# Performance work log

Hardware: AMD Instinct MI355X
Metric: run time of the kernel (lower is better)

The kernel has to match this reference:

```python
import jax, jax.numpy as jnp
import numpy as np

B, T, EMB, NDIM = 8, 2048, 1024, 1024


def setup_inputs() -> dict:
    key = jax.random.key(0)
    k1, k2, k3, k4 = jax.random.split(key, 4)
    X = jax.random.normal(k1, (B, T, EMB), dtype=jnp.float32)
    # Linear(emb, ndim, bias=False); stored as [emb, ndim] so projection is X @ W.
    scale = 1.0 / np.sqrt(EMB)
    Wq = jax.random.normal(k2, (EMB, NDIM), dtype=jnp.float32) * scale
    Wk = jax.random.normal(k3, (EMB, NDIM), dtype=jnp.float32) * scale
    Wv = jax.random.normal(k4, (EMB, NDIM), dtype=jnp.float32) * scale
    return {"X": X, "Wq": Wq, "Wk": Wk, "Wv": Wv}


def reference(X, Wq, Wk, Wv):
    ndim = Wq.shape[-1]
    T_ = X.shape[1]
    Q = X @ Wq  # [B,T,ndim]
    K = X @ Wk  # [B,T,ndim]
    V = X @ Wv  # [B,T,ndim]
    # scores[b,t,s] = Q[b,t] . K[b,s], scaled by ndim^-0.5
    scores = jnp.einsum("btd,bsd->bts", Q, K) * (ndim ** -0.5)
    mask = jnp.tril(jnp.ones((T_, T_), dtype=bool))  # causal lower-triangular
    scores = jnp.where(mask, scores, -jnp.inf)
    # NOTE: source uses F.softmax(..., dim=1) -> normalize over the QUERY axis
    # (columns of the [T,T] matrix), not the usual key axis. Replicated faithfully.
    probs = jax.nn.softmax(scores, axis=1)
    # dropout is identity in eval / p=0 deterministic baseline
    return probs @ V  # [B,T,ndim]
```

## Files before the change

kernel.cpp:

```cpp
#include <hip/hip_runtime.h>
#include <hip/hip_bf16.h>

#define B_   8
#define T_   2048
#define EMB_ 1024
#define ND_  1024
#define NTB  16
#define NPAIR 136
#define NTB2 8
#define NPAIR2 36

typedef __attribute__((ext_vector_type(8))) short   bf8_t;
typedef __attribute__((ext_vector_type(4))) float   f32x4;

__device__ __forceinline__ unsigned short f2bf(float f) {
  union { float f; unsigned int u; } c; c.f = f;
  unsigned int u = c.u;
  unsigned int r = (u + 0x7FFFu + ((u >> 16) & 1u)) >> 16;
  return (unsigned short)r;
}

__device__ __forceinline__ float bf2f(unsigned short b) {
  union { unsigned int u; float f; } c; c.u = ((unsigned int)b) << 16;
  return c.f;
}

__device__ __forceinline__ void gload_lds16(const unsigned short* g, unsigned short* l) {
  __builtin_amdgcn_global_load_lds(
      (const __attribute__((address_space(1))) unsigned int*)g,
      (__attribute__((address_space(3))) unsigned int*)l,
      16, 0, 0);
}

__device__ __forceinline__ void tri_decode(int p, int& tblk, int& sblk) {
  int t = (int)((sqrtf(8.0f * (float)p + 1.0f) - 1.0f) * 0.5f);
  while ((t + 1) * (t + 2) / 2 <= p) ++t;
  while (t * (t + 1) / 2 > p) --t;
  tblk = t;
  sblk = p - t * (t + 1) / 2;
}

#define SB0() __builtin_amdgcn_sched_barrier(0)
#define BAR() __builtin_amdgcn_s_barrier()

__device__ __forceinline__ void stage_half(const unsigned short* __restrict__ g, int lda,
                                           unsigned short* lhalf, int wave, int lane) {
  const int r3 = lane >> 3, c3 = lane & 7;
  const int colsw = ((c3 ^ r3) << 3);
#pragma unroll
  for (int j = 0; j < 2; ++j) {
    const int row = wave * 8 + r3 + 64 * j;
    gload_lds16(g + (size_t)row * lda + colsw, lhalf + wave * 512 + j * 4096);
  }
}

__device__ __forceinline__ bf8_t read_frag(const unsigned short* half, int r, int ks, int lane) {
  const int col = (((ks) << 5) + ((lane >> 4) << 3)) ^ ((r & 7) << 3);
  return *(const bf8_t*)(half + r * 64 + col);
}

__global__ void __launch_bounds__(256) cvt_x_kernel(const float* __restrict__ in,
                                                    unsigned short* __restrict__ out) {
  const int i = (blockIdx.x * 256 + threadIdx.x) * 4;
  float4 v = *(const float4*)(in + i);
  ushort4 o = make_ushort4(f2bf(v.x), f2bf(v.y), f2bf(v.z), f2bf(v.w));
  *(ushort4*)(out + i) = o;
}

__global__ void __launch_bounds__(256) transpose_w_kernel(const float* __restrict__ W,
                                                          unsigned short* __restrict__ Wt,
                                                          float cscale) {
  __shared__ unsigned short tile[32][33];
  const int n0 = blockIdx.x * 32, k0 = blockIdx.y * 32;
  const int tx = threadIdx.x & 31, ty = threadIdx.x >> 5;
#pragma unroll
  for (int r = 0; r < 32; r += 8) {
    float v = W[(size_t)(k0 + ty + r) * ND_ + n0 + tx];
    tile[tx][ty + r] = f2bf(v * cscale);
  }
  __syncthreads();
#pragma unroll
  for (int r = 0; r < 32; r += 8) {
    Wt[(size_t)(n0 + ty + r) * EMB_ + k0 + tx] = tile[ty + r][tx];
  }
}

#define LDSA(d, h) (lds256 + ((d) * 2 + (h)) * 8192)
#define LDSB(d, h) (lds256 + 32768 + ((d) * 2 + (h)) * 8192)

#define MFMA_QUAD(MB, AF, AOFF) do { \
  __builtin_amdgcn_s_setprio(1); \
  _Pragma("unroll") \
  for (int mi = 0; mi < 2; ++mi) \
    _Pragma("unroll") \
    for (int nf = 0; nf < 4; ++nf) \
      _Pragma("unroll") \
      for (int ks = 0; ks < 2; ++ks) \
        acc[(MB) * 2 + mi][nf] = __builtin_amdgcn_mfma_f32_16x16x32_bf16( \
            (AF)[(AOFF) + mi][ks], bfr[nf][ks], acc[(MB) * 2 + mi][nf], 0, 0, 0); \
  __builtin_amdgcn_s_setprio(0); \
} while (0)

#define GEMM256_LOOP(ABASE, BBASE, LDK) \
  stage_half((ABASE),                           (LDK), LDSA(0, 0), wave, lane); \
  stage_half((ABASE) + (size_t)128 * (LDK),     (LDK), LDSA(0, 1), wave, lane); \
  stage_half((BBASE),                           (LDK), LDSB(0, 0), wave, lane); \
  stage_half((BBASE) + (size_t)128 * (LDK),     (LDK), LDSB(0, 1), wave, lane); \
  stage_half((BBASE) + 64,                      (LDK), LDSB(1, 0), wave, lane); \
  stage_half((BBASE) + (size_t)128 * (LDK) + 64,(LDK), LDSB(1, 1), wave, lane); \
  stage_half((ABASE) + 64,                      (LDK), LDSA(1, 0), wave, lane); \
  asm volatile("s_waitcnt vmcnt(6)" ::: "memory"); \
  SB0(); BAR(); SB0(); \
  for (int t = 0; t < 16; ++t) { \
    const int d = t & 1; \
    const unsigned short* Ah = LDSA(d, wm); \
    const unsigned short* Bh = LDSB(d, wn >> 1); \
    bf8_t bfr[4][2], af[4][2]; \
    _Pragma("unroll") \
    for (int nf = 0; nf < 4; ++nf) \
      _Pragma("unroll") \
      for (int ks = 0; ks < 2; ++ks) bfr[nf][ks] = read_frag(Bh, brow + nf * 16, ks, lane); \
    _Pragma("unroll") \
    for (int mf = 0; mf < 4; ++mf) \
      _Pragma("unroll") \
      for (int ks = 0; ks < 2; ++ks) af[mf][ks] = read_frag(Ah, arow + mf * 16, ks, lane); \
    SB0(); \
    if (t < 15) stage_half((ABASE) + (size_t)128 * (LDK) + (size_t)(t + 1) * 64, (LDK), LDSA(d ^ 1, 1), wave, lane); \
    SB0(); BAR(); SB0(); \
    MFMA_QUAD(0, af, 0); \
    SB0(); \
    asm volatile("s_waitcnt lgkmcnt(0)" ::: "memory"); \
    SB0(); BAR(); SB0(); \
    if (t < 14) stage_half((BBASE) + (size_t)(t + 2) * 64, (LDK), LDSB(d, 0), wave, lane); \
    SB0(); BAR(); SB0(); \
    MFMA_QUAD(1, af, 2); \
    SB0(); BAR(); SB0(); \
    bf8_t af2[4][2]; \
    _Pragma("unroll") \
    for (int mf = 0; mf < 4; ++mf) \
      _Pragma("unroll") \
      for (int ks = 0; ks < 2; ++ks) af2[mf][ks] = read_frag(Ah, arow + (mf + 4) * 16, ks, lane); \
    SB0(); \
    if (t < 14) stage_half((BBASE) + (size_t)128 * (LDK) + (size_t)(t + 2) * 64, (LDK), LDSB(d, 1), wave, lane); \
    SB0(); BAR(); SB0(); \
    MFMA_QUAD(2, af2, 0); \
    SB0(); \
    asm volatile("s_waitcnt lgkmcnt(0)" ::: "memory"); \
    SB0(); BAR(); SB0(); \
    if (t < 14) stage_half((ABASE) + (size_t)(t + 2) * 64, (LDK), LDSA(d, 0), wave, lane); \
    if (t < 14)      { asm volatile("s_waitcnt vmcnt(6)" ::: "memory"); } \
    else if (t == 14){ asm volatile("s_waitcnt vmcnt(0)" ::: "memory"); } \
    SB0(); BAR(); SB0(); \
    MFMA_QUAD(3, af2, 2); \
    SB0(); BAR(); SB0(); \
  }

template <int OUTMODE>
__global__ void __launch_bounds__(512, 2)
gemm_xw256_kernel(const unsigned short* __restrict__ A,
                  const unsigned short* __restrict__ Bt,
                  unsigned short* __restrict__ C) {
  extern __shared__ unsigned short lds256[];
  const int tid = threadIdx.x, lane = tid & 63, wave = tid >> 6;
  const int wm = wave >> 2, wn = wave & 3;
  const int m0 = blockIdx.y * 256, n0 = blockIdx.x * 256;
  const unsigned short* Ab = A + (size_t)m0 * EMB_;
  const unsigned short* Bb = Bt + (size_t)n0 * EMB_;
  f32x4 acc[8][4];
#pragma unroll
  for (int i = 0; i < 8; ++i)
#pragma unroll
    for (int j = 0; j < 4; ++j)
#pragma unroll
      for (int q = 0; q < 4; ++q) acc[i][j][q] = 0.f;
  const int arow = lane & 15;
  const int brow = (wn & 1) * 64 + (lane & 15);

  GEMM256_LOOP(Ab, Bb, EMB_)

  const int cc = lane & 15, cr4 = (lane >> 4) << 2;
#pragma unroll
  for (int mf = 0; mf < 8; ++mf)
#pragma unroll
    for (int nf = 0; nf < 4; ++nf)
#pragma unroll
      for (int q = 0; q < 4; ++q) {
        const int row = m0 + wm * 128 + mf * 16 + cr4 + q;
        const int col = n0 + wn * 64 + nf * 16 + cc;
        const unsigned short val = f2bf(acc[mf][nf][q]);
        if (OUTMODE == 0) {
          C[(size_t)row * ND_ + col] = val;
        } else {
          const int bb = row >> 11, tt = row & 2047;
          C[((size_t)bb * ND_ + col) * T_ + tt] = val;
        }
      }
}

__global__ void __launch_bounds__(512, 2)
scoretile256_kernel(const unsigned short* __restrict__ Qb,
                    const unsigned short* __restrict__ Kb,
                    unsigned short* __restrict__ Sb,
                    float* __restrict__ pm,
                    float* __restrict__ pl) {
  extern __shared__ unsigned short lds256[];
  int tr, sr;
  tri_decode(blockIdx.x, tr, sr);
  const int b = blockIdx.y;
  const int tid = threadIdx.x, lane = tid & 63, wave = tid >> 6;
  const int wm = wave >> 2, wn = wave & 3;
  const int t0 = tr * 256, s0 = sr * 256;
  const unsigned short* Ab = Qb + ((size_t)b * T_ + t0) * ND_;
  const unsigned short* Bb = Kb + ((size_t)b * T_ + s0) * ND_;
  f32x4 acc[8][4];
#pragma unroll
  for (int i = 0; i < 8; ++i)
#pragma unroll
    for (int j = 0; j < 4; ++j)
#pragma unroll
      for (int q = 0; q < 4; ++q) acc[i][j][q] = 0.f;
  const int arow = lane & 15;
  const int brow = (wn & 1) * 64 + (lane & 15);

  GEMM256_LOOP(Ab, Bb, ND_)

  const int cc = lane & 15, cr4 = (lane >> 4) << 2;
  const bool diag = (tr == sr);
  unsigned short* Sbase = Sb + (size_t)b * T_ * T_;
  float rm[4], rl[4];
#pragma unroll
  for (int nf = 0; nf < 4; ++nf) { rm[nf] = -1e30f; rl[nf] = 0.f; }
#pragma unroll
  for (int mf = 0; mf < 8; ++mf)
#pragma unroll
    for (int nf = 0; nf < 4; ++nf)
#pragma unroll
      for (int q = 0; q < 4; ++q) {
        const int t = t0 + wm * 128 + mf * 16 + cr4 + q;
        const int s = s0 + wn * 64 + nf * 16 + cc;
        const bool ok = !diag || (t >= s);
        const unsigned short bv = ok ? f2bf(acc[mf][nf][q]) : (unsigned short)0;
        Sbase[(size_t)t * T_ + s] = bv;
        if (ok) {
          const float v = bf2f(bv);
          const float mm = fmaxf(rm[nf], v);
          rl[nf] = rl[nf] * __expf(rm[nf] - mm) + __expf(v - mm);
          rm[nf] = mm;
        }
      }
#pragma unroll
  for (int nf = 0; nf < 4; ++nf) {
#pragma unroll
    for (int off = 16; off < 64; off <<= 1) {
      const float om = __shfl_xor(rm[nf], off);
      const float ol = __shfl_xor(rl[nf], off);
      const float mm = fmaxf(rm[nf], om);
      rl[nf] = rl[nf] * __expf(rm[nf] - mm) + ol * __expf(om - mm);
      rm[nf] = mm;
    }
  }
  __syncthreads();
  float* red = (float*)lds256;
  if (lane < 16) {
#pragma unroll
    for (int nf = 0; nf < 4; ++nf) {
      red[((wm * 4 + wn) * 4 + nf) * 16 + lane] = rm[nf];
      red[512 + ((wm * 4 + wn) * 4 + nf) * 16 + lane] = rl[nf];
    }
  }
  __syncthreads();
  if (wm == 0 && lane < 16) {
    const size_t base = (((size_t)b * NTB2 + sr) * NTB2 + tr) * 256;
#pragma unroll
    for (int nf = 0; nf < 4; ++nf) {
      const float m0v = red[((0 * 4 + wn) * 4 + nf) * 16 + lane];
      const float l0v = red[512 + ((0 * 4 + wn) * 4 + nf) * 16 + lane];
      const float m1v = red[((1 * 4 + wn) * 4 + nf) * 16 + lane];
      const float l1v = red[512 + ((1 * 4 + wn) * 4 + nf) * 16 + lane];
      const float mm = fmaxf(m0v, m1v);
      const float ll = l0v * __expf(m0v - mm) + l1v * __expf(m1v - mm);
      pm[base + wn * 64 + nf * 16 + lane] = mm;
      pl[base + wn * 64 + nf * 16 + lane] = ll;
    }
  }
}

__global__ void __launch_bounds__(256) colreduce_kernel(const float* __restrict__ pm,
                                                        const float* __restrict__ pl,
                                                        float* __restrict__ colmax,
                                                        float* __restrict__ colinv) {
  const int sr = blockIdx.x, b = blockIdx.y, c = threadIdx.x;
  float m = -1e30f, l = 0.f;
  for (int tr = sr; tr < NTB2; ++tr) {
    const size_t base = (((size_t)b * NTB2 + sr) * NTB2 + tr) * 256;
    const float om = pm[base + c], ol = pl[base + c];
    const float mm = fmaxf(m, om);
    l = l * __expf(m - mm) + ol * __expf(om - mm);
    m = mm;
  }
  colmax[(size_t)b * T_ + sr * 256 + c] = m;
  colinv[(size_t)b * T_ + sr * 256 + c] = 1.0f / l;
}

__global__ void __launch_bounds__(256) pscale_kernel(unsigned short* __restrict__ Pb,
                                                     const float* __restrict__ colmax,
                                                     const float* __restrict__ colinv) {
  int tblk, sblk;
  tri_decode(blockIdx.x, tblk, sblk);
  const int b = blockIdx.y;
  const int s0 = sblk * 128, t0 = tblk * 128;
  const int tid = threadIdx.x;
  const int col8 = (tid & 15) * 8;
  const int rbase = tid >> 4;
  unsigned short* Pbase = Pb + (size_t)b * T_ * T_;
  float ms[8], inv[8];
#pragma unroll
  for (int j = 0; j < 8; ++j) {
    ms[j]  = colmax[(size_t)b * T_ + s0 + col8 + j];
    inv[j] = colinv[(size_t)b * T_ + s0 + col8 + j];
  }
  const bool diag = (tblk == sblk);
  for (int r = rbase; r < 128; r += 16) {
    const int t = t0 + r;
    unsigned short* p = Pbase + (size_t)t * T_ + s0 + col8;
    bf8_t v = *(bf8_t*)p;
#pragma unroll
    for (int j = 0; j < 8; ++j) {
      float pv = 0.f;
      if (!diag || t >= s0 + col8 + j) {
        pv = __expf(bf2f((unsigned short)v[j]) - ms[j]) * inv[j];
      }
      v[j] = (short)f2bf(pv);
    }
    *(bf8_t*)p = v;
  }
}

#define MFMA_Q8(MB) do { \
  __builtin_amdgcn_s_setprio(1); \
  _Pragma("unroll") \
  for (int nf = 0; nf < 4; ++nf) \
    _Pragma("unroll") \
    for (int ks = 0; ks < 2; ++ks) \
      acc[(MB)][nf] = __builtin_amdgcn_mfma_f32_16x16x32_bf16( \
          af[(MB)][ks], bfr[nf][ks], acc[(MB)][nf], 0, 0, 0); \
  __builtin_amdgcn_s_setprio(0); \
} while (0)

__device__ __forceinline__ void pv_segment(const unsigned short* __restrict__ Ab,
                                           const unsigned short* __restrict__ Bb,
                                           float* __restrict__ Cb,
                                           int ktiles, unsigned short* lds256,
                                           int lane, int wave) {
  const int wm = wave >> 2, wn = wave & 3;
  const int arow = lane & 15;
  f32x4 acc[4][4];
#pragma unroll
  for (int i = 0; i < 4; ++i)
#pragma unroll
    for (int j = 0; j < 4; ++j)
#pragma unroll
      for (int q = 0; q < 4; ++q) acc[i][j][q] = 0.f;

  stage_half(Ab,                           T_, lds256,                     wave, lane);
  stage_half(Bb,                           T_, lds256 + 16384,             wave, lane);
  stage_half(Bb + (size_t)128 * T_,        T_, lds256 + 16384 + 8192,      wave, lane);
  stage_half(Ab + 64,                      T_, lds256 + 8192,              wave, lane);
  stage_half(Bb + 64,                      T_, lds256 + 16384 + 2 * 8192,  wave, lane);
  stage_half(Bb + (size_t)128 * T_ + 64,   T_, lds256 + 16384 + 3 * 8192,  wave, lane);
  asm volatile("s_waitcnt vmcnt(6)" ::: "memory");
  SB0(); BAR(); SB0();

  for (int t = 0; t < ktiles; ++t) {
    const int d = t & 1;
    const unsigned short* Ah = lds256 + d * 8192;
    const unsigned short* Bh = lds256 + 16384 + (d * 2 + (wn >> 1)) * 8192;
    bf8_t bfr[4][2], af[4][2];
#pragma unroll
    for (int nf = 0; nf < 4; ++nf)
#pragma unroll
      for (int ks = 0; ks < 2; ++ks)
        bfr[nf][ks] = read_frag(Bh, (wn & 1) * 64 + nf * 16 + arow, ks, lane);
#pragma unroll
    for (int mf = 0; mf < 4; ++mf)
#pragma unroll
      for (int ks = 0; ks < 2; ++ks)
        af[mf][ks] = read_frag(Ah, wm * 64 + mf * 16 + arow, ks, lane);
    SB0(); BAR(); SB0();
    MFMA_Q8(0);
    SB0();
    asm volatile("s_waitcnt lgkmcnt(0)" ::: "memory");
    SB0(); BAR(); SB0();
    if (t < ktiles - 2) stage_half(Ab + (size_t)(t + 2) * 64, T_, lds256 + d * 8192, wave, lane);
    SB0(); BAR(); SB0();
    MFMA_Q8(1);
    SB0(); BAR(); SB0();
    if (t < ktiles - 2) stage_half(Bb + (size_t)(t + 2) * 64, T_, lds256 + 16384 + (d * 2) * 8192, wave, lane);
    SB0(); BAR(); SB0();
    MFMA_Q8(2);
    SB0(); BAR(); SB0();
    if (t < ktiles - 2) stage_half(Bb + (size_t)128 * T_ + (size_t)(t + 2) * 64, T_, lds256 + 16384 + (d * 2 + 1) * 8192, wave, lane);
    if (t < ktiles - 2)      { asm volatile("s_waitcnt vmcnt(6)" ::: "memory"); }
    else if (t == ktiles - 2){ asm volatile("s_waitcnt vmcnt(0)" ::: "memory"); }
    SB0(); BAR(); SB0();
    MFMA_Q8(3);
    SB0(); BAR(); SB0();
  }

  const int cc = lane & 15, cr4 = (lane >> 4) << 2;
#pragma unroll
  for (int mf = 0; mf < 4; ++mf)
#pragma unroll
    for (int nf = 0; nf < 4; ++nf)
#pragma unroll
      for (int q = 0; q < 4; ++q) {
        const int row = wm * 64 + mf * 16 + cr4 + q;
        const int col = wn * 64 + nf * 16 + cc;
        Cb[(size_t)row * ND_ + col] = acc[mf][nf][q];
      }
}

__global__ void __launch_bounds__(512, 2)
gemm_pv256_kernel(const unsigned short* __restrict__ Pb,
                  const unsigned short* __restrict__ Vt,
                  float* __restrict__ out) {
  extern __shared__ unsigned short lds256[];
  const int pair = blockIdx.x;
  const int ncol = blockIdx.y;
  const int b = blockIdx.z;
  const int tid = threadIdx.x, lane = tid & 63, wave = tid >> 6;
  const int tbs[2] = {pair, 15 - pair};
#pragma unroll
  for (int si = 0; si < 2; ++si) {
    const int tb = tbs[si];
    const int ktiles = 2 * tb + 2;
    pv_segment(Pb + (size_t)b * T_ * T_ + (size_t)tb * 128 * T_,
               Vt + (size_t)b * ND_ * T_ + (size_t)ncol * 256 * T_,
               out + (size_t)b * T_ * ND_ + (size_t)tb * 128 * ND_ + ncol * 256,
               ktiles, lds256, lane, wave);
  }
}

extern "C" void kernel_launch(void* const* d_in, const int* in_sizes, int n_in,
                              void* d_out, int out_size, void* d_ws, size_t ws_size,
                              hipStream_t stream) {
  const float* X  = (const float*)d_in[0];
  const float* Wq = (const float*)d_in[1];
  const float* Wk = (const float*)d_in[2];
  const float* Wv = (const float*)d_in[3];
  float* out = (float*)d_out;
  (void)in_sizes; (void)n_in; (void)out_size;

  char* ws = (char*)d_ws;
  size_t off = 0;
  auto alloc = [&](size_t bytes) {
    void* p = ws + off;
    off += (bytes + 255) & ~(size_t)255;
    return p;
  };
  unsigned short* Xb  = (unsigned short*)alloc((size_t)B_ * T_ * EMB_ * 2);
  unsigned short* Wtq = (unsigned short*)alloc((size_t)ND_ * EMB_ * 2);
  unsigned short* Wtk = (unsigned short*)alloc((size_t)ND_ * EMB_ * 2);
  unsigned short* Wtv = (unsigned short*)alloc((size_t)ND_ * EMB_ * 2);
  unsigned short* Qb  = (unsigned short*)alloc((size_t)B_ * T_ * ND_ * 2);
  unsigned short* Kb  = (unsigned short*)alloc((size_t)B_ * T_ * ND_ * 2);
  unsigned short* Vt  = (unsigned short*)alloc((size_t)B_ * ND_ * T_ * 2);
  float* colmax = (float*)alloc((size_t)B_ * T_ * 4);
  float* colinv = (float*)alloc((size_t)B_ * T_ * 4);
  float* pm     = (float*)alloc((size_t)B_ * NTB2 * NTB2 * 256 * 4);
  float* pl     = (float*)alloc((size_t)B_ * NTB2 * NTB2 * 256 * 4);
  unsigned short* Pb  = (unsigned short*)alloc((size_t)B_ * T_ * T_ * 2);
  if (off > ws_size) return;

  hipFuncSetAttribute((const void*)&gemm_xw256_kernel<0>,
                      hipFuncAttributeMaxDynamicSharedMemorySize, 131072);
  hipFuncSetAttribute((const void*)&gemm_xw256_kernel<1>,
                      hipFuncAttributeMaxDynamicSharedMemorySize, 131072);
  hipFuncSetAttribute((const void*)&scoretile256_kernel,
                      hipFuncAttributeMaxDynamicSharedMemorySize, 131072);
  hipFuncSetAttribute((const void*)&gemm_pv256_kernel,
                      hipFuncAttributeMaxDynamicSharedMemorySize, 98304);

  hipLaunchKernelGGL(cvt_x_kernel, dim3((B_ * T_ * EMB_) / 1024), dim3(256), 0, stream, X, Xb);
  hipLaunchKernelGGL(transpose_w_kernel, dim3(32, 32), dim3(256), 0, stream, Wq, Wtq, 0.03125f);
  hipLaunchKernelGGL(transpose_w_kernel, dim3(32, 32), dim3(256), 0, stream, Wk, Wtk, 1.0f);
  hipLaunchKernelGGL(transpose_w_kernel, dim3(32, 32), dim3(256), 0, stream, Wv, Wtv, 1.0f);
  hipLaunchKernelGGL((gemm_xw256_kernel<0>), dim3(ND_ / 256, (B_ * T_) / 256), dim3(512), 131072, stream, Xb, Wtq, Qb);
  hipLaunchKernelGGL((gemm_xw256_kernel<0>), dim3(ND_ / 256, (B_ * T_) / 256), dim3(512), 131072, stream, Xb, Wtk, Kb);
  hipLaunchKernelGGL((gemm_xw256_kernel<1>), dim3(ND_ / 256, (B_ * T_) / 256), dim3(512), 131072, stream, Xb, Wtv, Vt);
  hipLaunchKernelGGL(scoretile256_kernel, dim3(NPAIR2, B_), dim3(512), 131072, stream, Qb, Kb, Pb, pm, pl);
  hipLaunchKernelGGL(colreduce_kernel, dim3(NTB2, B_), dim3(256), 0, stream, pm, pl, colmax, colinv);
  hipLaunchKernelGGL(pscale_kernel, dim3(NPAIR, B_), dim3(256), 0, stream, Pb, colmax, colinv);
  hipLaunchKernelGGL(gemm_pv256_kernel, dim3(NTB2, ND_ / 256, B_), dim3(512), 98304, stream, Pb, Vt, out);
}
```

Measured before the change: 305.2 us.

## Stage GEMM epilogues through swizzled LDS, reschedule prefetches, remap grid order

The GEMM and score-tile epilogues now write bf16 results into swizzled LDS first and then store them to global memory as coalesced 16-byte vectors. This replaces scattered 2-byte stores, including the strided transposed V output. The prefetch schedule in the XW GEMM and PV loops is regrouped: A and B half-tiles are issued in pairs, waitcnt thresholds change, and all of the first A tile is loaded in the prologue. The score and PV grids are flattened so batch becomes the fastest-varying block index, which changes how blocks are spread across CUs and how they share cache. The risks are an extra barrier plus an LDS round trip, and heavier bursts of loads at each stage point.

After: 302.4 us. No clear change (-0.9%).

```diff
diff --git a/kernel.cpp b/kernel.cpp
--- a/kernel.cpp
+++ b/kernel.cpp
@@ -58,6 +58,8 @@
   const int col = (((ks) << 5) + ((lane >> 4) << 3)) ^ ((r & 7) << 3);
   return *(const bf8_t*)(half + r * 64 + col);
 }
+
+__device__ __forceinline__ int swz_ep(int x) { return ((x >> 1) & 7) << 4; }
 
 __global__ void __launch_bounds__(256) cvt_x_kernel(const float* __restrict__ in,
                                                     unsigned short* __restrict__ out) {
@@ -102,14 +104,15 @@
 } while (0)
 
 #define GEMM256_LOOP(ABASE, BBASE, LDK) \
-  stage_half((ABASE),                           (LDK), LDSA(0, 0), wave, lane); \
-  stage_half((ABASE) + (size_t)128 * (LDK),     (LDK), LDSA(0, 1), wave, lane); \
-  stage_half((BBASE),                           (LDK), LDSB(0, 0), wave, lane); \
-  stage_half((BBASE) + (size_t)128 * (LDK),     (LDK), LDSB(0, 1), wave, lane); \
-  stage_half((BBASE) + 64,                      (LDK), LDSB(1, 0), wave, lane); \
-  stage_half((BBASE) + (size_t)128 * (LDK) + 64,(LDK), LDSB(1, 1), wave, lane); \
-  stage_half((ABASE) + 64,                      (LDK), LDSA(1, 0), wave, lane); \
-  asm volatile("s_waitcnt vmcnt(6)" ::: "memory"); \
+  stage_half((ABASE),                             (LDK), LDSA(0, 0), wave, lane); \
+  stage_half((ABASE) + (size_t)128 * (LDK),       (LDK), LDSA(0, 1), wave, lane); \
+  stage_half((BBASE),                             (LDK), LDSB(0, 0), wave, lane); \
+  stage_half((BBASE) + (size_t)128 * (LDK),       (LDK), LDSB(0, 1), wave, lane); \
+  stage_half((BBASE) + 64,                        (LDK), LDSB(1, 0), wave, lane); \
+  stage_half((BBASE) + (size_t)128 * (LDK) + 64,  (LDK), LDSB(1, 1), wave, lane); \
+  stage_half((ABASE) + 64,                        (LDK), LDSA(1, 0), wave, lane); \
+  stage_half((ABASE) + (size_t)128 * (LDK) + 64,  (LDK), LDSA(1, 1), wave, lane); \
+  asm volatile("s_waitcnt vmcnt(8)" ::: "memory"); \
   SB0(); BAR(); SB0(); \
   for (int t = 0; t < 16; ++t) { \
     const int d = t & 1; \
@@ -124,14 +127,15 @@
     for (int mf = 0; mf < 4; ++mf) \
       _Pragma("unroll") \
       for (int ks = 0; ks < 2; ++ks) af[mf][ks] = read_frag(Ah, arow + mf * 16, ks, lane); \
-    SB0(); \
-    if (t < 15) stage_half((ABASE) + (size_t)128 * (LDK) + (size_t)(t + 1) * 64, (LDK), LDSA(d ^ 1, 1), wave, lane); \
     SB0(); BAR(); SB0(); \
     MFMA_QUAD(0, af, 0); \
     SB0(); \
     asm volatile("s_waitcnt lgkmcnt(0)" ::: "memory"); \
     SB0(); BAR(); SB0(); \
-    if (t < 14) stage_half((BBASE) + (size_t)(t + 2) * 64, (LDK), LDSB(d, 0), wave, lane); \
+    if (t < 14) { \
+      stage_half((BBASE) + (size_t)(t + 2) * 64,                     (LDK), LDSB(d, 0), wave, lane); \
+      stage_half((BBASE) + (size_t)128 * (LDK) + (size_t)(t + 2) * 64,(LDK), LDSB(d, 1), wave, lane); \
+    } \
     SB0(); BAR(); SB0(); \
     MFMA_QUAD(1, af, 2); \
     SB0(); BAR(); SB0(); \
@@ -140,20 +144,44 @@
     for (int mf = 0; mf < 4; ++mf) \
       _Pragma("unroll") \
       for (int ks = 0; ks < 2; ++ks) af2[mf][ks] = read_frag(Ah, arow + (mf + 4) * 16, ks, lane); \
-    SB0(); \
-    if (t < 14) stage_half((BBASE) + (size_t)128 * (LDK) + (size_t)(t + 2) * 64, (LDK), LDSB(d, 1), wave, lane); \
     SB0(); BAR(); SB0(); \
     MFMA_QUAD(2, af2, 0); \
     SB0(); \
     asm volatile("s_waitcnt lgkmcnt(0)" ::: "memory"); \
     SB0(); BAR(); SB0(); \
-    if (t < 14) stage_half((ABASE) + (size_t)(t + 2) * 64, (LDK), LDSA(d, 0), wave, lane); \
-    if (t < 14)      { asm volatile("s_waitcnt vmcnt(6)" ::: "memory"); } \
-    else if (t == 14){ asm volatile("s_waitcnt vmcnt(0)" ::: "memory"); } \
+    if (t < 14) { \
+      stage_half((ABASE) + (size_t)(t + 2) * 64,                     (LDK), LDSA(d, 0), wave, lane); \
+      stage_half((ABASE) + (size_t)128 * (LDK) + (size_t)(t + 2) * 64,(LDK), LDSA(d, 1), wave, lane); \
+      asm volatile("s_waitcnt vmcnt(8)" ::: "memory"); \
+    } else if (t == 14) { \
+      asm volatile("s_waitcnt vmcnt(0)" ::: "memory"); \
+    } \
     SB0(); BAR(); SB0(); \
     MFMA_QUAD(3, af2, 2); \
     SB0(); BAR(); SB0(); \
   }
+
+#define ACC_TO_LDS(TRANS, MASKED) do { \
+  _Pragma("unroll") \
+  for (int mf = 0; mf < 8; ++mf) \
+    _Pragma("unroll") \
+    for (int nf = 0; nf < 4; ++nf) \
+      _Pragma("unroll") \
+      for (int q = 0; q < 4; ++q) { \
+        const int r = wm * 128 + mf * 16 + cr4 + q; \
+        const int c = wn * 64 + nf * 16 + cc; \
+        unsigned short bv; \
+        if (MASKED) { \
+          const bool ok = !diag || (t0 + r >= s0 + c); \
+          bv = ok ? f2bf(acc[mf][nf][q]) : (unsigned short)0; \
+        } else { \
+          bv = f2bf(acc[mf][nf][q]); \
+        } \
+        const int byte = (TRANS) ? (c * 512 + ((r * 2) ^ swz_ep(c))) \
+                                 : (r * 512 + ((c * 2) ^ swz_ep(r))); \
+        lds256[byte >> 1] = bv; \
+      } \
+} while (0)
 
 template <int OUTMODE>
 __global__ void __launch_bounds__(512, 2)
@@ -179,22 +207,27 @@
   GEMM256_LOOP(Ab, Bb, EMB_)
 
   const int cc = lane & 15, cr4 = (lane >> 4) << 2;
-#pragma unroll
-  for (int mf = 0; mf < 8; ++mf)
-#pragma unroll
-    for (int nf = 0; nf < 4; ++nf)
-#pragma unroll
-      for (int q = 0; q < 4; ++q) {
-        const int row = m0 + wm * 128 + mf * 16 + cr4 + q;
-        const int col = n0 + wn * 64 + nf * 16 + cc;
-        const unsigned short val = f2bf(acc[mf][nf][q]);
-        if (OUTMODE == 0) {
-          C[(size_t)row * ND_ + col] = val;
-        } else {
-          const int bb = row >> 11, tt = row & 2047;
-          C[((size_t)bb * ND_ + col) * T_ + tt] = val;
-        }
-      }
+  const bool diag = false; const int t0 = 0, s0 = 0; (void)diag; (void)t0; (void)s0;
+  ACC_TO_LDS(OUTMODE == 1, false);
+  __syncthreads();
+  if (OUTMODE == 0) {
+#pragma unroll
+    for (int p = 0; p < 16; ++p) {
+      const int o = p * 8192 + tid * 16;
+      const int ri = o >> 9, cb = o & 511;
+      const bf8_t v = *(const bf8_t*)(lds256 + (((o & ~511) | (cb ^ swz_ep(ri))) >> 1));
+      *(bf8_t*)(C + (size_t)(m0 + ri) * ND_ + n0 + (cb >> 1)) = v;
+    }
+  } else {
+    const int bb = m0 >> 11, tt0 = m0 & 2047;
+#pragma unroll
+    for (int p = 0; p < 16; ++p) {
+      const int o = p * 8192 + tid * 16;
+      const int ci = o >> 9, rb = o & 511;
+      const bf8_t v = *(const bf8_t*)(lds256 + (((o & ~511) | (rb ^ swz_ep(ci))) >> 1));
+      *(bf8_t*)(C + ((size_t)bb * ND_ + n0 + ci) * T_ + tt0 + (rb >> 1)) = v;
+    }
+  }
 }
 
 __global__ void __launch_bounds__(512, 2)
@@ -204,9 +237,9 @@
                     float* __restrict__ pm,
                     float* __restrict__ pl) {
   extern __shared__ unsigned short lds256[];
+  const int b = blockIdx.x & 7;
   int tr, sr;
-  tri_decode(blockIdx.x, tr, sr);
-  const int b = blockIdx.y;
+  tri_decode(blockIdx.x >> 3, tr, sr);
   const int tid = threadIdx.x, lane = tid & 63, wave = tid >> 6;
   const int wm = wave >> 2, wn = wave & 3;
   const int t0 = tr * 256, s0 = sr * 256;
@@ -226,7 +259,6 @@
 
   const int cc = lane & 15, cr4 = (lane >> 4) << 2;
   const bool diag = (tr == sr);
-  unsigned short* Sbase = Sb + (size_t)b * T_ * T_;
   float rm[4], rl[4];
 #pragma unroll
   for (int nf = 0; nf < 4; ++nf) { rm[nf] = -1e30f; rl[nf] = 0.f; }
@@ -236,11 +268,11 @@
     for (int nf = 0; nf < 4; ++nf)
 #pragma unroll
       for (int q = 0; q < 4; ++q) {
-        const int t = t0 + wm * 128 + mf * 16 + cr4 + q;
-        const int s = s0 + wn * 64 + nf * 16 + cc;
-        const bool ok = !diag || (t >= s);
+        const int r = wm * 128 + mf * 16 + cr4 + q;
+        const int c = wn * 64 + nf * 16 + cc;
+        const bool ok = !diag || (t0 + r >= s0 + c);
         const unsigned short bv = ok ? f2bf(acc[mf][nf][q]) : (unsigned short)0;
-        Sbase[(size_t)t * T_ + s] = bv;
+        lds256[(r * 512 + ((c * 2) ^ swz_ep(r))) >> 1] = bv;
         if (ok) {
           const float v = bf2f(bv);
           const float mm = fmaxf(rm[nf], v);
@@ -248,6 +280,15 @@
           rm[nf] = mm;
         }
       }
+  __syncthreads();
+  unsigned short* Sbase = Sb + (size_t)b * T_ * T_;
+#pragma unroll
+  for (int p = 0; p < 16; ++p) {
+    const int o = p * 8192 + tid * 16;
+    const int ri = o >> 9, cb = o & 511;
+    const bf8_t v = *(const bf8_t*)(lds256 + (((o & ~511) | (cb ^ swz_ep(ri))) >> 1));
+    *(bf8_t*)(Sbase + (size_t)(t0 + ri) * T_ + s0 + (cb >> 1)) = v;
+  }
 #pragma unroll
   for (int nf = 0; nf < 4; ++nf) {
 #pragma unroll
@@ -391,15 +432,18 @@
     SB0();
     asm volatile("s_waitcnt lgkmcnt(0)" ::: "memory");
     SB0(); BAR(); SB0();
-    if (t < ktiles - 2) stage_half(Ab + (size_t)(t + 2) * 64, T_, lds256 + d * 8192, wave, lane);
+    if (t < ktiles - 2) {
+      stage_half(Ab + (size_t)(t + 2) * 64, T_, lds256 + d * 8192, wave, lane);
+      stage_half(Bb + (size_t)(t + 2) * 64, T_, lds256 + 16384 + (d * 2) * 8192, wave, lane);
+    }
     SB0(); BAR(); SB0();
     MFMA_Q8(1);
     SB0(); BAR(); SB0();
-    if (t < ktiles - 2) stage_half(Bb + (size_t)(t + 2) * 64, T_, lds256 + 16384 + (d * 2) * 8192, wave, lane);
+    if (t < ktiles - 2)
+      stage_half(Bb + (size_t)128 * T_ + (size_t)(t + 2) * 64, T_, lds256 + 16384 + (d * 2 + 1) * 8192, wave, lane);
     SB0(); BAR(); SB0();
     MFMA_Q8(2);
     SB0(); BAR(); SB0();
-    if (t < ktiles - 2) stage_half(Bb + (size_t)128 * T_ + (size_t)(t + 2) * 64, T_, lds256 + 16384 + (d * 2 + 1) * 8192, wave, lane);
     if (t < ktiles - 2)      { asm volatile("s_waitcnt vmcnt(6)" ::: "memory"); }
     else if (t == ktiles - 2){ asm volatile("s_waitcnt vmcnt(0)" ::: "memory"); }
     SB0(); BAR(); SB0();
@@ -425,9 +469,9 @@
                   const unsigned short* __restrict__ Vt,
                   float* __restrict__ out) {
   extern __shared__ unsigned short lds256[];
-  const int pair = blockIdx.x;
-  const int ncol = blockIdx.y;
-  const int b = blockIdx.z;
+  const int b = blockIdx.x & 7;
+  const int pair = (blockIdx.x >> 3) & 7;
+  const int ncol = blockIdx.x >> 6;
   const int tid = threadIdx.x, lane = tid & 63, wave = tid >> 6;
   const int tbs[2] = {pair, 15 - pair};
 #pragma unroll
@@ -488,8 +532,8 @@
   hipLaunchKernelGGL((gemm_xw256_kernel<0>), dim3(ND_ / 256, (B_ * T_) / 256), dim3(512), 131072, stream, Xb, Wtq, Qb);
   hipLaunchKernelGGL((gemm_xw256_kernel<0>), dim3(ND_ / 256, (B_ * T_) / 256), dim3(512), 131072, stream, Xb, Wtk, Kb);
   hipLaunchKernelGGL((gemm_xw256_kernel<1>), dim3(ND_ / 256, (B_ * T_) / 256), dim3(512), 131072, stream, Xb, Wtv, Vt);
-  hipLaunchKernelGGL(scoretile256_kernel, dim3(NPAIR2, B_), dim3(512), 131072, stream, Qb, Kb, Pb, pm, pl);
+  hipLaunchKernelGGL(scoretile256_kernel, dim3(NPAIR2 * B_), dim3(512), 131072, stream, Qb, Kb, Pb, pm, pl);
   hipLaunchKernelGGL(colreduce_kernel, dim3(NTB2, B_), dim3(256), 0, stream, pm, pl, colmax, colinv);
   hipLaunchKernelGGL(pscale_kernel, dim3(NPAIR, B_), dim3(256), 0, stream, Pb, colmax, colinv);
-  hipLaunchKernelGGL(gemm_pv256_kernel, dim3(NTB2, ND_ / 256, B_), dim3(512), 98304, stream, Pb, Vt, out);
-}
+  hipLaunchKernelGGL(gemm_pv256_kernel, dim3(NTB2 * 4 * B_), dim3(512), 98304, stream, Pb, Vt, out);
+}
```
